# Kernel tuning notes

Measured on AMD Instinct MI355X. Metric: run time of the kernel, lower is better.

## Reference

```python
import jax, jax.numpy as jnp
import numpy as np

VOC = 32000
D = 512          # embedding_dim == hidden_dim
POS = 1024       # position_embeddings_count


def _layernorm(x, gamma, beta, eps=1e-5):
    mu = jnp.mean(x, axis=-1, keepdims=True)
    var = jnp.var(x, axis=-1, keepdims=True)
    return (x - mu) * jax.lax.rsqrt(var + eps) * gamma + beta


def setup_inputs() -> dict:
    key = jax.random.key(0)
    ks = jax.random.split(key, 7)
    inp = jax.random.randint(ks[0], (32, 1024), 0, VOC)
    word_emb = jax.random.normal(ks[1], (VOC, D), dtype=jnp.float32) * 0.02
    pos_emb = jax.random.normal(ks[2], (POS, D), dtype=jnp.float32) * 0.02
    gamma = jnp.ones((D,), dtype=jnp.float32)
    beta = jnp.zeros((D,), dtype=jnp.float32)
    # torch.rand -> uniform [0,1) init in the original Attention module
    Wk = jax.random.uniform(ks[3], (D, D), dtype=jnp.float32)
    Wq = jax.random.uniform(ks[4], (D, D), dtype=jnp.float32)
    Wv = jax.random.uniform(ks[5], (D, D), dtype=jnp.float32)
    return {"input": inp, "word_emb": word_emb, "pos_emb": pos_emb,
            "gamma": gamma, "beta": beta, "Wk": Wk, "Wq": Wq, "Wv": Wv}


def reference(input, word_emb, pos_emb, gamma, beta, Wk, Wq, Wv):
    S = input.shape[-1]
    # MiniBertEmbedding: word + positional, then LayerNorm
    emb = word_emb[input] + pos_emb[:S][None, :, :]   # [B,S,D]
    x = _layernorm(emb, gamma, beta)
    # Attention: single-head QK^T softmax V with param matrices
    k = jnp.einsum('bsd,dh->bsh', x, Wk)
    q = jnp.einsum('bsd,dh->bsh', x, Wq)
    v = jnp.einsum('bsd,do->bso', x, Wv)
    qk = jnp.einsum('bqh,bkh->bqk', q, k) / jnp.sqrt(jnp.float32(D))
    attn = jax.nn.softmax(qk, axis=-1)
    return jnp.einsum('bqk,bko->bqo', attn, v)
```

## Files before the change

### kernel.cpp

```cpp
#include <hip/hip_runtime.h>
#include <math.h>

typedef _Float16 f16;
typedef _Float16 half8 __attribute__((ext_vector_type(8)));
typedef _Float16 hv2 __attribute__((ext_vector_type(2)));
typedef _Float16 hv4 __attribute__((ext_vector_type(4)));
typedef float f32x4 __attribute__((ext_vector_type(4)));
typedef __attribute__((address_space(1))) const unsigned int gu32;
typedef __attribute__((address_space(3))) unsigned int lu32;

#define BB 32
#define SS 1024
#define DD 512
#define NR (BB*SS)
#define CH 16

__device__ __forceinline__ void stage128(const char* g, int ldb, char* lds,
                                         int wv, int ln) {
  #pragma unroll
  for (int r = 0; r < 4; r++) {
    int slot = r * 256 + wv * 64 + ln;
    int row = slot >> 3, cp = slot & 7;
    int c = cp ^ (row & 7);
    const char* gp = g + (size_t)row * ldb + (c << 4);
    char* lp = lds + ((slot - ln) << 4);
    __builtin_amdgcn_global_load_lds((gu32*)gp, (lu32*)lp, 16, 0, 0);
  }
}

__device__ __forceinline__ void stage8k_512(const char* g, int ldb, char* lds) {
  int tid = threadIdx.x;
  int slot = tid;
  int row = slot >> 3, cp = slot & 7;
  int c = cp ^ (row & 7);
  const char* gp = g + (size_t)row * ldb + (c << 4);
  char* lp = lds + ((slot - (tid & 63)) << 4);
  __builtin_amdgcn_global_load_lds((gu32*)gp, (lu32*)lp, 16, 0, 0);
}

__device__ __forceinline__ half8 frag_ld(const char* lds, int row, int kc) {
  return *(const half8*)(lds + row * 128 + ((kc ^ (row & 7)) << 4));
}

__device__ __forceinline__ f32x4 MF(half8 a, half8 b, f32x4 c) {
  return __builtin_amdgcn_mfma_f32_16x16x32_f16(a, b, c, 0, 0, 0);
}

__global__ __launch_bounds__(256) void k_prep(
    const int* __restrict__ inp, const float* __restrict__ wemb,
    const float* __restrict__ pemb, const float* __restrict__ gamma,
    const float* __restrict__ beta, f16* __restrict__ Xhi, f16* __restrict__ Xlo,
    const float* __restrict__ Wq, const float* __restrict__ Wk,
    const float* __restrict__ Wv, f16* __restrict__ Wqh, f16* __restrict__ Wql,
    f16* __restrict__ Wkh, f16* __restrict__ Wkl, f16* __restrict__ Wvt)
{
  int bid = blockIdx.x;
  int tid = threadIdx.x;
  __shared__ float red[10];
  __shared__ float Lt[64][65];
  if (bid >= NR) {
    int t  = bid - NR;
    int mz = t >> 6;
    int tt = t & 63;
    if (mz < 2) {
      const float* W = mz ? Wk : Wq;
      f16* Oh = mz ? Wkh : Wqh;
      f16* Ol = mz ? Wkl : Wql;
      #pragma unroll
      for (int p = 0; p < 4; p++) {
        size_t base = (size_t)tt * 4096 + p * 1024 + tid * 4;
        float4 v = *(const float4*)&W[base];
        f16 h0 = (f16)v.x, h1 = (f16)v.y, h2 = (f16)v.z, h3 = (f16)v.w;
        hv4 hi = {h0, h1, h2, h3};
        hv4 lo = {(f16)(v.x - (float)h0), (f16)(v.y - (float)h1),
                  (f16)(v.z - (float)h2), (f16)(v.w - (float)h3)};
        *(hv4*)&Oh[base] = hi;
        *(hv4*)&Ol[base] = lo;
      }
      return;
    }
    int tr = tt >> 3, tc = tt & 7;
    int rr = tid >> 4;
    int c4 = (tid & 15) * 4;
    #pragma unroll
    for (int p = 0; p < 4; p++) {
      float4 v = *(const float4*)&Wv[(size_t)(tr * 64 + p * 16 + rr) * DD + tc * 64 + c4];
      Lt[p * 16 + rr][c4 + 0] = v.x; Lt[p * 16 + rr][c4 + 1] = v.y;
      Lt[p * 16 + rr][c4 + 2] = v.z; Lt[p * 16 + rr][c4 + 3] = v.w;
    }
    __syncthreads();
    #pragma unroll
    for (int p = 0; p < 4; p++) {
      int dl = p * 16 + rr;
      float v0 = Lt[c4 + 0][dl], v1 = Lt[c4 + 1][dl];
      float v2 = Lt[c4 + 2][dl], v3 = Lt[c4 + 3][dl];
      size_t o = (size_t)(tc * 64 + dl) * DD + tr * 64 + c4;
      *(hv4*)&Wvt[o] = (hv4){(f16)v0, (f16)v1, (f16)v2, (f16)v3};
    }
    return;
  }
  int row = bid;
  int s   = row & (SS - 1);
  int tok = inp[row];
  float2 w = ((const float2*)(wemb + (size_t)tok * DD))[tid];
  float2 p = ((const float2*)(pemb + (size_t)s   * DD))[tid];
  float ex = w.x + p.x, ey = w.y + p.y;
  float sum = ex + ey, ssq = ex*ex + ey*ey;
  #pragma unroll
  for (int off = 32; off > 0; off >>= 1) {
    sum += __shfl_down(sum, off, 64);
    ssq += __shfl_down(ssq, off, 64);
  }
  int wv = tid >> 6, ln = tid & 63;
  if (ln == 0) { red[wv] = sum; red[4 + wv] = ssq; }
  __syncthreads();
  if (tid == 0) {
    float s4 = red[0] + red[1] + red[2] + red[3];
    float q4 = red[4] + red[5] + red[6] + red[7];
    float mean = s4 * (1.0f / DD);
    float var  = q4 * (1.0f / DD) - mean * mean;
    red[8] = mean; red[9] = rsqrtf(var + 1e-5f);
  }
  __syncthreads();
  float mean = red[8], rstd = red[9];
  float2 g  = ((const float2*)gamma)[tid];
  float2 bt = ((const float2*)beta)[tid];
  float ox = (ex - mean) * rstd * g.x + bt.x;
  float oy = (ey - mean) * rstd * g.y + bt.y;
  f16 hx = (f16)ox, hy = (f16)oy;
  f16 lx = (f16)(ox - (float)hx), ly = (f16)(oy - (float)hy);
  ((hv2*)(Xhi + (size_t)row * DD))[tid] = (hv2){hx, hy};
  ((hv2*)(Xlo + (size_t)row * DD))[tid] = (hv2){lx, ly};
}

__global__ __launch_bounds__(256, 2) void k_mt(
    const f16* __restrict__ Wkh, const f16* __restrict__ Wkl,
    const f16* __restrict__ Wqh, const f16* __restrict__ Wql,
    f16* __restrict__ Mthi, f16* __restrict__ Mtlo)
{
  __shared__ __align__(16) char Ah[16384], Al[16384], Bh[16384], Bl[16384];
  int tid = threadIdx.x, wv = tid >> 6, ln = tid & 63;
  int mw = wv & 1, nw = wv >> 1;
  int n0 = blockIdx.x * 128;
  int m0 = blockIdx.y * 128;
  f32x4 acc[4][4];
  #pragma unroll
  for (int i = 0; i < 4; i++)
    #pragma unroll
    for (int j = 0; j < 4; j++) acc[i][j] = (f32x4)(0.0f);
  int quad = ln >> 4, l15 = ln & 15;
  for (int k0 = 0; k0 < DD; k0 += 64) {
    __syncthreads();
    stage128((const char*)(Wkh + (size_t)m0 * DD + k0), 1024, Ah, wv, ln);
    stage128((const char*)(Wkl + (size_t)m0 * DD + k0), 1024, Al, wv, ln);
    stage128((const char*)(Wqh + (size_t)n0 * DD + k0), 1024, Bh, wv, ln);
    stage128((const char*)(Wql + (size_t)n0 * DD + k0), 1024, Bl, wv, ln);
    __syncthreads();
    #pragma unroll
    for (int ks = 0; ks < 2; ks++) {
      int kc = ks * 4 + quad;
      half8 ah[4], al[4], bh[4], bl[4];
      #pragma unroll
      for (int t = 0; t < 4; t++) {
        ah[t] = frag_ld(Ah, mw * 64 + t * 16 + l15, kc);
        al[t] = frag_ld(Al, mw * 64 + t * 16 + l15, kc);
        bh[t] = frag_ld(Bh, nw * 64 + t * 16 + l15, kc);
        bl[t] = frag_ld(Bl, nw * 64 + t * 16 + l15, kc);
      }
      #pragma unroll
      for (int i = 0; i < 4; i++)
        #pragma unroll
        for (int j = 0; j < 4; j++) {
          acc[i][j] = MF(ah[i], bh[j], acc[i][j]);
          acc[i][j] = MF(ah[i], bl[j], acc[i][j]);
          acc[i][j] = MF(al[i], bh[j], acc[i][j]);
        }
    }
  }
  #pragma unroll
  for (int i = 0; i < 4; i++)
    #pragma unroll
    for (int j = 0; j < 4; j++)
      #pragma unroll
      for (int rg = 0; rg < 4; rg++) {
        int gm = m0 + mw * 64 + i * 16 + quad * 4 + rg;
        int gn = n0 + nw * 64 + j * 16 + l15;
        size_t o = (size_t)gm * DD + gn;
        float v = acc[i][j][rg];
        f16 h = (f16)v;
        Mthi[o] = h; Mtlo[o] = (f16)(v - (float)h);
      }
}

__global__ __launch_bounds__(256, 2) void k_projm(
    const f16* __restrict__ Xhi, const f16* __restrict__ Xlo,
    const f16* __restrict__ Mthi, const f16* __restrict__ Mtlo,
    f16* __restrict__ Sqhi, f16* __restrict__ Sqlo)
{
  __shared__ __align__(16) char Ah[16384], Al[16384], Bh[16384], Bl[16384];
  int tid = threadIdx.x, wv = tid >> 6, ln = tid & 63;
  int mw = wv & 1, nw = wv >> 1;
  int L = blockIdx.x;
  int xb = (L >> 3) & 3;
  int y  = ((L >> 5) << 3) + (L & 7);
  int n0 = xb * 128;
  int m0 = y * 128;
  f32x4 acc[4][4];
  #pragma unroll
  for (int i = 0; i < 4; i++)
    #pragma unroll
    for (int j = 0; j < 4; j++) acc[i][j] = (f32x4)(0.0f);
  int quad = ln >> 4, l15 = ln & 15;
  for (int k0 = 0; k0 < DD; k0 += 64) {
    __syncthreads();
    stage128((const char*)(Xhi  + (size_t)m0 * DD + k0), 1024, Ah, wv, ln);
    stage128((const char*)(Xlo  + (size_t)m0 * DD + k0), 1024, Al, wv, ln);
    stage128((const char*)(Mthi + (size_t)n0 * DD + k0), 1024, Bh, wv, ln);
    stage128((const char*)(Mtlo + (size_t)n0 * DD + k0), 1024, Bl, wv, ln);
    __syncthreads();
    #pragma unroll
    for (int ks = 0; ks < 2; ks++) {
      int kc = ks * 4 + quad;
      half8 ah[4], al[4], bh[4], bl[4];
      #pragma unroll
      for (int t = 0; t < 4; t++) {
        ah[t] = frag_ld(Ah, mw * 64 + t * 16 + l15, kc);
        al[t] = frag_ld(Al, mw * 64 + t * 16 + l15, kc);
        bh[t] = frag_ld(Bh, nw * 64 + t * 16 + l15, kc);
        bl[t] = frag_ld(Bl, nw * 64 + t * 16 + l15, kc);
      }
      #pragma unroll
      for (int i = 0; i < 4; i++)
        #pragma unroll
        for (int j = 0; j < 4; j++) {
          acc[i][j] = MF(ah[i], bh[j], acc[i][j]);
          acc[i][j] = MF(ah[i], bl[j], acc[i][j]);
          acc[i][j] = MF(al[i], bh[j], acc[i][j]);
        }
    }
  }
  #pragma unroll
  for (int i = 0; i < 4; i++)
    #pragma unroll
    for (int j = 0; j < 4; j++)
      #pragma unroll
      for (int rg = 0; rg < 4; rg++) {
        int gm = m0 + mw * 64 + i * 16 + quad * 4 + rg;
        int gn = n0 + nw * 64 + j * 16 + l15;
        size_t o = (size_t)gm * DD + gn;
        float v = acc[i][j][rg];
        f16 h = (f16)v;
        Sqhi[o] = h; Sqlo[o] = (f16)(v - (float)h);
      }
}

__global__ __launch_bounds__(256, 2) void k_vt(
    const f16* __restrict__ Wvt, const f16* __restrict__ Xhi, f16* __restrict__ Vt)
{
  __shared__ __align__(16) char Ah[16384], Bh[16384];
  int tid = threadIdx.x, wv = tid >> 6, ln = tid & 63;
  int mw = wv & 1, nw = wv >> 1;
  int n0 = blockIdx.x * 128;
  int m0 = blockIdx.y * 128;
  f32x4 acc[4][4];
  #pragma unroll
  for (int i = 0; i < 4; i++)
    #pragma unroll
    for (int j = 0; j < 4; j++) acc[i][j] = (f32x4)(0.0f);
  for (int k0 = 0; k0 < DD; k0 += 64) {
    __syncthreads();
    stage128((const char*)(Wvt + (size_t)m0 * DD + k0), 1024, Ah, wv, ln);
    stage128((const char*)(Xhi + (size_t)n0 * DD + k0), 1024, Bh, wv, ln);
    __syncthreads();
    int quad = ln >> 4, l15 = ln & 15;
    #pragma unroll
    for (int ks = 0; ks < 2; ks++) {
      int kc = ks * 4 + quad;
      half8 a[4], b[4];
      #pragma unroll
      for (int t = 0; t < 4; t++) {
        a[t] = frag_ld(Ah, mw * 64 + t * 16 + l15, kc);
        b[t] = frag_ld(Bh, nw * 64 + t * 16 + l15, kc);
      }
      #pragma unroll
      for (int i = 0; i < 4; i++)
        #pragma unroll
        for (int j = 0; j < 4; j++) acc[i][j] = MF(a[i], b[j], acc[i][j]);
    }
  }
  int quad = ln >> 4, l15 = ln & 15;
  #pragma unroll
  for (int i = 0; i < 4; i++)
    #pragma unroll
    for (int j = 0; j < 4; j++)
      #pragma unroll
      for (int rg = 0; rg < 4; rg++) {
        int gm = m0 + mw * 64 + i * 16 + quad * 4 + rg;
        int gn = n0 + nw * 64 + j * 16 + l15;
        Vt[(size_t)gm * NR + gn] = (f16)acc[i][j][rg];
      }
}

__global__ __launch_bounds__(512, 2) void k_qk(
    const f16* __restrict__ Sqhi, const f16* __restrict__ Sqlo,
    const f16* __restrict__ Xhi, const f16* __restrict__ Xlo,
    f16* __restrict__ Pws, f16* __restrict__ Pd)
{
  __shared__ __align__(16) char Ah[8192], Al[8192];
  __shared__ __align__(16) char Bh[2][4][8192], Bl[2][4][8192];
  __shared__ float redm[4][64], reds[4][64];
  int tid = threadIdx.x, wv = tid >> 6, ln = tid & 63;
  int rowg = wv & 1, qd = wv >> 1;
  int L = blockIdx.x;
  int g  = L >> 7;
  int rr = L & 127;
  int z  = g * 8 + (rr & 7);
  int m0 = (rr >> 3) * 64;
  size_t zr = (size_t)z * SS;
  f32x4 acc[2][16];
  #pragma unroll
  for (int i = 0; i < 2; i++)
    #pragma unroll
    for (int j = 0; j < 16; j++) acc[i][j] = (f32x4)(0.0f);
  int quad = ln >> 4, l15 = ln & 15;

  #pragma unroll
  for (int q4 = 0; q4 < 4; q4++) {
    stage8k_512((const char*)(Xhi + (zr + q4 * 256) * DD), 1024, Bh[0][q4]);
    stage8k_512((const char*)(Xlo + (zr + q4 * 256) * DD), 1024, Bl[0][q4]);
  }

  for (int k0 = 0; k0 < DD; k0 += 64) {
    #pragma unroll
    for (int r = 0; r < 4; r++) {
      __builtin_amdgcn_s_barrier();
      __builtin_amdgcn_sched_barrier(0);
      if (r == 0) {
        stage8k_512((const char*)(Sqhi + (zr + m0) * DD + k0), 1024, Ah);
        stage8k_512((const char*)(Sqlo + (zr + m0) * DD + k0), 1024, Al);
      }
      bool haveNext = !(k0 == DD - 64 && r == 3);
      if (haveNext) {
        int nk0 = (r == 3) ? k0 + 64 : k0;
        int nr  = (r + 1) & 3;
        #pragma unroll
        for (int q4 = 0; q4 < 4; q4++) {
          int n0 = q4 * 256 + nr * 64;
          stage8k_512((const char*)(Xhi + (zr + n0) * DD + nk0), 1024, Bh[(r + 1) & 1][q4]);
          stage8k_512((const char*)(Xlo + (zr + n0) * DD + nk0), 1024, Bl[(r + 1) & 1][q4]);
        }
        asm volatile("s_waitcnt vmcnt(8)" ::: "memory");
      } else {
        asm volatile("s_waitcnt vmcnt(0)" ::: "memory");
      }
      __builtin_amdgcn_s_barrier();
      __builtin_amdgcn_sched_barrier(0);
      #pragma unroll
      for (int ks = 0; ks < 2; ks++) {
        int kc = ks * 4 + quad;
        half8 ah[2], al[2];
        #pragma unroll
        for (int i = 0; i < 2; i++) {
          ah[i] = frag_ld(Ah, rowg * 32 + i * 16 + l15, kc);
          al[i] = frag_ld(Al, rowg * 32 + i * 16 + l15, kc);
        }
        #pragma unroll
        for (int jj = 0; jj < 4; jj++) {
          half8 bh = frag_ld(Bh[r & 1][qd], jj * 16 + l15, kc);
          half8 bl = frag_ld(Bl[r & 1][qd], jj * 16 + l15, kc);
          #pragma unroll
          for (int i = 0; i < 2; i++) {
            acc[i][r * 4 + jj] = MF(ah[i], bh, acc[i][r * 4 + jj]);
            acc[i][r * 4 + jj] = MF(ah[i], bl, acc[i][r * 4 + jj]);
            acc[i][r * 4 + jj] = MF(al[i], bh, acc[i][r * 4 + jj]);
          }
        }
      }
    }
  }

  const float scale = 0.044194173824159216f;
  float mx[2][4];
  #pragma unroll
  for (int i = 0; i < 2; i++)
    #pragma unroll
    for (int rg = 0; rg < 4; rg++) mx[i][rg] = -3.0e38f;
  #pragma unroll
  for (int i = 0; i < 2; i++)
    #pragma unroll
    for (int j = 0; j < 16; j++)
      #pragma unroll
      for (int rg = 0; rg < 4; rg++) {
        acc[i][j][rg] *= scale;
        mx[i][rg] = fmaxf(mx[i][rg], acc[i][j][rg]);
      }
  #pragma unroll
  for (int off = 1; off < 16; off <<= 1)
    #pragma unroll
    for (int i = 0; i < 2; i++)
      #pragma unroll
      for (int rg = 0; rg < 4; rg++)
        mx[i][rg] = fmaxf(mx[i][rg], __shfl_xor(mx[i][rg], off, 64));
  if (l15 == 0) {
    #pragma unroll
    for (int i = 0; i < 2; i++)
      #pragma unroll
      for (int rg = 0; rg < 4; rg++)
        redm[qd][rowg * 32 + i * 16 + quad * 4 + rg] = mx[i][rg];
  }
  __syncthreads();
  float fm[2][4], sum[2][4];
  #pragma unroll
  for (int i = 0; i < 2; i++)
    #pragma unroll
    for (int rg = 0; rg < 4; rg++) {
      int row = rowg * 32 + i * 16 + quad * 4 + rg;
      fm[i][rg] = fmaxf(fmaxf(redm[0][row], redm[1][row]),
                        fmaxf(redm[2][row], redm[3][row]));
      sum[i][rg] = 0.0f;
    }
  #pragma unroll
  for (int i = 0; i < 2; i++)
    #pragma unroll
    for (int j = 0; j < 16; j++)
      #pragma unroll
      for (int rg = 0; rg < 4; rg++) {
        float e = __expf(acc[i][j][rg] - fm[i][rg]);
        acc[i][j][rg] = e;
        sum[i][rg] += e;
      }
  #pragma unroll
  for (int off = 1; off < 16; off <<= 1)
    #pragma unroll
    for (int i = 0; i < 2; i++)
      #pragma unroll
      for (int rg = 0; rg < 4; rg++)
        sum[i][rg] += __shfl_xor(sum[i][rg], off, 64);
  if (l15 == 0) {
    #pragma unroll
    for (int i = 0; i < 2; i++)
      #pragma unroll
      for (int rg = 0; rg < 4; rg++)
        reds[qd][rowg * 32 + i * 16 + quad * 4 + rg] = sum[i][rg];
  }
  __syncthreads();
  float inv[2][4];
  #pragma unroll
  for (int i = 0; i < 2; i++)
    #pragma unroll
    for (int rg = 0; rg < 4; rg++) {
      int row = rowg * 32 + i * 16 + quad * 4 + rg;
      inv[i][rg] = 1.0f / (reds[0][row] + reds[1][row] + reds[2][row] + reds[3][row]);
    }
  f16* Pb = (z < CH) ? Pws : Pd;
  size_t zo = (size_t)((z < CH) ? z : z - CH);
  #pragma unroll
  for (int i = 0; i < 2; i++)
    #pragma unroll
    for (int j = 0; j < 16; j++)
      #pragma unroll
      for (int rg = 0; rg < 4; rg++) {
        int row = rowg * 32 + i * 16 + quad * 4 + rg;
        int col = qd * 256 + j * 16 + l15;
        Pb[(zo * SS + m0 + row) * SS + col] = (f16)(acc[i][j][rg] * inv[i][rg]);
      }
}

__global__ __launch_bounds__(256, 2) void k_pv(
    const f16* __restrict__ P, const f16* __restrict__ Vt, float* __restrict__ O,
    int zoff)
{
  __shared__ __align__(16) char Ah[16384], Bh[16384];
  int tid = threadIdx.x, wv = tid >> 6, ln = tid & 63;
  int mw = wv & 1, nw = wv >> 1;
  int n0 = blockIdx.x * 128;
  int m0 = blockIdx.y * 128;
  int zl = blockIdx.z;
  int b  = zoff + zl;
  const char* Pt = (const char*)(P + ((size_t)zl * SS + m0) * SS);
  f32x4 acc[4][4];
  #pragma unroll
  for (int i = 0; i < 4; i++)
    #pragma unroll
    for (int j = 0; j < 4; j++) acc[i][j] = (f32x4)(0.0f);
  for (int k0 = 0; k0 < SS; k0 += 64) {
    __syncthreads();
    stage128(Pt + k0 * 2, 2048, Ah, wv, ln);
    stage128((const char*)(Vt + (size_t)n0 * NR + (size_t)b * SS + k0), NR * 2, Bh, wv, ln);
    __syncthreads();
    int quad = ln >> 4, l15 = ln & 15;
    #pragma unroll
    for (int ks = 0; ks < 2; ks++) {
      int kc = ks * 4 + quad;
      half8 a[4], bf[4];
      #pragma unroll
      for (int t = 0; t < 4; t++) {
        a[t]  = frag_ld(Ah, mw * 64 + t * 16 + l15, kc);
        bf[t] = frag_ld(Bh, nw * 64 + t * 16 + l15, kc);
      }
      #pragma unroll
      for (int i = 0; i < 4; i++)
        #pragma unroll
        for (int j = 0; j < 4; j++) acc[i][j] = MF(a[i], bf[j], acc[i][j]);
    }
  }
  int quad = ln >> 4, l15 = ln & 15;
  #pragma unroll
  for (int i = 0; i < 4; i++)
    #pragma unroll
    for (int j = 0; j < 4; j++)
      #pragma unroll
      for (int rg = 0; rg < 4; rg++) {
        int gm = m0 + mw * 64 + i * 16 + quad * 4 + rg;
        int gn = n0 + nw * 64 + j * 16 + l15;
        O[((size_t)b * SS + gm) * DD + gn] = acc[i][j][rg];
      }
}

extern "C" void kernel_launch(void* const* d_in, const int* in_sizes, int n_in,
                              void* d_out, int out_size, void* d_ws, size_t ws_size,
                              hipStream_t stream) {
  const int*   inp   = (const int*)d_in[0];
  const float* wemb  = (const float*)d_in[1];
  const float* pemb  = (const float*)d_in[2];
  const float* gamma = (const float*)d_in[3];
  const float* beta  = (const float*)d_in[4];
  const float* Wk    = (const float*)d_in[5];
  const float* Wq    = (const float*)d_in[6];
  const float* Wv    = (const float*)d_in[7];

  char* ws = (char*)d_ws;
  f16* Xhi  = (f16*)ws;
  f16* Xlo  = (f16*)(ws + ((size_t)32 << 20));
  f16* Sqhi = (f16*)(ws + ((size_t)64 << 20));
  f16* Sqlo = (f16*)(ws + ((size_t)96 << 20));
  f16* Vt   = (f16*)(ws + ((size_t)128 << 20));
  f16* Pws  = (f16*)(ws + ((size_t)160 << 20));
  f16* Pd   = (f16*)d_out;

  f16* Wqh  = (f16*)d_out;
  f16* Wql  = Wqh + (size_t)DD * DD;
  f16* Wkh  = Wql + (size_t)DD * DD;
  f16* Wkl  = Wkh + (size_t)DD * DD;
  f16* Wvt  = Wkl + (size_t)DD * DD;
  f16* Mthi = Wvt + (size_t)DD * DD;
  f16* Mtlo = Mthi + (size_t)DD * DD;

  k_prep<<<NR + 192, 256, 0, stream>>>(inp, wemb, pemb, gamma, beta, Xhi, Xlo,
                                       Wq, Wk, Wv, Wqh, Wql, Wkh, Wkl, Wvt);
  k_mt<<<dim3(DD / 128, DD / 128), 256, 0, stream>>>(Wkh, Wkl, Wqh, Wql, Mthi, Mtlo);
  k_projm<<<1024, 256, 0, stream>>>(Xhi, Xlo, Mthi, Mtlo, Sqhi, Sqlo);
  k_vt<<<dim3(NR / 128, DD / 128), 256, 0, stream>>>(Wvt, Xhi, Vt);
  k_qk<<<512, 512, 0, stream>>>(Sqhi, Sqlo, Xhi, Xlo, Pws, Pd);
  k_pv<<<dim3(DD / 128, SS / 128, CH), 256, 0, stream>>>(Pd,  Vt, (float*)d_out, CH);
  k_pv<<<dim3(DD / 128, SS / 128, CH), 256, 0, stream>>>(Pws, Vt, (float*)d_out, 0);
}
```

Measured before the change: 424.4 us.

## Double-buffer LDS in k_vt/k_pv, remap blocks per XCD, hoist A fragments in k_qk

```diff
diff --git a/kernel.cpp b/kernel.cpp
--- a/kernel.cpp
+++ b/kernel.cpp
@@ -257,30 +257,43 @@
 __global__ __launch_bounds__(256, 2) void k_vt(
     const f16* __restrict__ Wvt, const f16* __restrict__ Xhi, f16* __restrict__ Vt)
 {
-  __shared__ __align__(16) char Ah[16384], Bh[16384];
+  __shared__ __align__(16) char Ah[2][16384], Bh[2][16384];
   int tid = threadIdx.x, wv = tid >> 6, ln = tid & 63;
   int mw = wv & 1, nw = wv >> 1;
-  int n0 = blockIdx.x * 128;
-  int m0 = blockIdx.y * 128;
+  int orig = blockIdx.x;
+  int L = (orig & 7) * 128 + (orig >> 3);
+  int c = L >> 7, t = L & 127;
+  int m0 = (t & 3) * 128;
+  int n0 = (c * 32 + (t >> 2)) * 128;
   f32x4 acc[4][4];
   #pragma unroll
   for (int i = 0; i < 4; i++)
     #pragma unroll
     for (int j = 0; j < 4; j++) acc[i][j] = (f32x4)(0.0f);
+  int quad = ln >> 4, l15 = ln & 15;
+  stage128((const char*)(Wvt + (size_t)m0 * DD), 1024, Ah[0], wv, ln);
+  stage128((const char*)(Xhi + (size_t)n0 * DD), 1024, Bh[0], wv, ln);
   for (int k0 = 0; k0 < DD; k0 += 64) {
-    __syncthreads();
-    stage128((const char*)(Wvt + (size_t)m0 * DD + k0), 1024, Ah, wv, ln);
-    stage128((const char*)(Xhi + (size_t)n0 * DD + k0), 1024, Bh, wv, ln);
-    __syncthreads();
-    int quad = ln >> 4, l15 = ln & 15;
+    int cur = (k0 >> 6) & 1;
+    __builtin_amdgcn_s_barrier();
+    __builtin_amdgcn_sched_barrier(0);
+    if (k0 + 64 < DD) {
+      stage128((const char*)(Wvt + (size_t)m0 * DD + k0 + 64), 1024, Ah[cur ^ 1], wv, ln);
+      stage128((const char*)(Xhi + (size_t)n0 * DD + k0 + 64), 1024, Bh[cur ^ 1], wv, ln);
+      asm volatile("s_waitcnt vmcnt(8)" ::: "memory");
+    } else {
+      asm volatile("s_waitcnt vmcnt(0)" ::: "memory");
+    }
+    __builtin_amdgcn_s_barrier();
+    __builtin_amdgcn_sched_barrier(0);
     #pragma unroll
     for (int ks = 0; ks < 2; ks++) {
       int kc = ks * 4 + quad;
       half8 a[4], b[4];
       #pragma unroll
-      for (int t = 0; t < 4; t++) {
-        a[t] = frag_ld(Ah, mw * 64 + t * 16 + l15, kc);
-        b[t] = frag_ld(Bh, nw * 64 + t * 16 + l15, kc);
+      for (int tt = 0; tt < 4; tt++) {
+        a[tt] = frag_ld(Ah[cur], mw * 64 + tt * 16 + l15, kc);
+        b[tt] = frag_ld(Bh[cur], nw * 64 + tt * 16 + l15, kc);
       }
       #pragma unroll
       for (int i = 0; i < 4; i++)
@@ -288,7 +301,6 @@
         for (int j = 0; j < 4; j++) acc[i][j] = MF(a[i], b[j], acc[i][j]);
     }
   }
-  int quad = ln >> 4, l15 = ln & 15;
   #pragma unroll
   for (int i = 0; i < 4; i++)
     #pragma unroll
@@ -330,6 +342,7 @@
     stage8k_512((const char*)(Xlo + (zr + q4 * 256) * DD), 1024, Bl[0][q4]);
   }
 
+  half8 afh[2][2], afl[2][2];
   for (int k0 = 0; k0 < DD; k0 += 64) {
     #pragma unroll
     for (int r = 0; r < 4; r++) {
@@ -355,24 +368,27 @@
       }
       __builtin_amdgcn_s_barrier();
       __builtin_amdgcn_sched_barrier(0);
+      if (r == 0) {
+        #pragma unroll
+        for (int ks = 0; ks < 2; ks++)
+          #pragma unroll
+          for (int i = 0; i < 2; i++) {
+            afh[ks][i] = frag_ld(Ah, rowg * 32 + i * 16 + l15, ks * 4 + quad);
+            afl[ks][i] = frag_ld(Al, rowg * 32 + i * 16 + l15, ks * 4 + quad);
+          }
+      }
       #pragma unroll
       for (int ks = 0; ks < 2; ks++) {
         int kc = ks * 4 + quad;
-        half8 ah[2], al[2];
-        #pragma unroll
-        for (int i = 0; i < 2; i++) {
-          ah[i] = frag_ld(Ah, rowg * 32 + i * 16 + l15, kc);
-          al[i] = frag_ld(Al, rowg * 32 + i * 16 + l15, kc);
-        }
         #pragma unroll
         for (int jj = 0; jj < 4; jj++) {
           half8 bh = frag_ld(Bh[r & 1][qd], jj * 16 + l15, kc);
           half8 bl = frag_ld(Bl[r & 1][qd], jj * 16 + l15, kc);
           #pragma unroll
           for (int i = 0; i < 2; i++) {
-            acc[i][r * 4 + jj] = MF(ah[i], bh, acc[i][r * 4 + jj]);
-            acc[i][r * 4 + jj] = MF(ah[i], bl, acc[i][r * 4 + jj]);
-            acc[i][r * 4 + jj] = MF(al[i], bh, acc[i][r * 4 + jj]);
+            acc[i][r * 4 + jj] = MF(afh[ks][i], bh, acc[i][r * 4 + jj]);
+            acc[i][r * 4 + jj] = MF(afh[ks][i], bl, acc[i][r * 4 + jj]);
+            acc[i][r * 4 + jj] = MF(afl[ks][i], bh, acc[i][r * 4 + jj]);
           }
         }
       }
@@ -470,33 +486,47 @@
     const f16* __restrict__ P, const f16* __restrict__ Vt, float* __restrict__ O,
     int zoff)
 {
-  __shared__ __align__(16) char Ah[16384], Bh[16384];
+  __shared__ __align__(16) char Ah[2][16384], Bh[2][16384];
   int tid = threadIdx.x, wv = tid >> 6, ln = tid & 63;
   int mw = wv & 1, nw = wv >> 1;
-  int n0 = blockIdx.x * 128;
-  int m0 = blockIdx.y * 128;
-  int zl = blockIdx.z;
+  int orig = blockIdx.x;
+  int L = (orig & 7) * 64 + (orig >> 3);
+  int c = L >> 6, t = L & 63;
+  int zl = 2 * c + (t >> 5);
+  int m0 = ((t >> 2) & 7) * 128;
+  int n0 = (t & 3) * 128;
   int b  = zoff + zl;
   const char* Pt = (const char*)(P + ((size_t)zl * SS + m0) * SS);
+  const char* Vb = (const char*)(Vt + (size_t)n0 * NR + (size_t)b * SS);
   f32x4 acc[4][4];
   #pragma unroll
   for (int i = 0; i < 4; i++)
     #pragma unroll
     for (int j = 0; j < 4; j++) acc[i][j] = (f32x4)(0.0f);
+  int quad = ln >> 4, l15 = ln & 15;
+  stage128(Pt, 2048, Ah[0], wv, ln);
+  stage128(Vb, NR * 2, Bh[0], wv, ln);
   for (int k0 = 0; k0 < SS; k0 += 64) {
-    __syncthreads();
-    stage128(Pt + k0 * 2, 2048, Ah, wv, ln);
-    stage128((const char*)(Vt + (size_t)n0 * NR + (size_t)b * SS + k0), NR * 2, Bh, wv, ln);
-    __syncthreads();
-    int quad = ln >> 4, l15 = ln & 15;
+    int cur = (k0 >> 6) & 1;
+    __builtin_amdgcn_s_barrier();
+    __builtin_amdgcn_sched_barrier(0);
+    if (k0 + 64 < SS) {
+      stage128(Pt + (k0 + 64) * 2, 2048, Ah[cur ^ 1], wv, ln);
+      stage128(Vb + (k0 + 64) * 2, NR * 2, Bh[cur ^ 1], wv, ln);
+      asm volatile("s_waitcnt vmcnt(8)" ::: "memory");
+    } else {
+      asm volatile("s_waitcnt vmcnt(0)" ::: "memory");
+    }
+    __builtin_amdgcn_s_barrier();
+    __builtin_amdgcn_sched_barrier(0);
     #pragma unroll
     for (int ks = 0; ks < 2; ks++) {
       int kc = ks * 4 + quad;
       half8 a[4], bf[4];
       #pragma unroll
-      for (int t = 0; t < 4; t++) {
-        a[t]  = frag_ld(Ah, mw * 64 + t * 16 + l15, kc);
-        bf[t] = frag_ld(Bh, nw * 64 + t * 16 + l15, kc);
+      for (int tt = 0; tt < 4; tt++) {
+        a[tt]  = frag_ld(Ah[cur], mw * 64 + tt * 16 + l15, kc);
+        bf[tt] = frag_ld(Bh[cur], nw * 64 + tt * 16 + l15, kc);
       }
       #pragma unroll
       for (int i = 0; i < 4; i++)
@@ -504,7 +534,6 @@
         for (int j = 0; j < 4; j++) acc[i][j] = MF(a[i], bf[j], acc[i][j]);
     }
   }
-  int quad = ln >> 4, l15 = ln & 15;
   #pragma unroll
   for (int i = 0; i < 4; i++)
     #pragma unroll
@@ -550,8 +579,8 @@
                                        Wq, Wk, Wv, Wqh, Wql, Wkh, Wkl, Wvt);
   k_mt<<<dim3(DD / 128, DD / 128), 256, 0, stream>>>(Wkh, Wkl, Wqh, Wql, Mthi, Mtlo);
   k_projm<<<1024, 256, 0, stream>>>(Xhi, Xlo, Mthi, Mtlo, Sqhi, Sqlo);
-  k_vt<<<dim3(NR / 128, DD / 128), 256, 0, stream>>>(Wvt, Xhi, Vt);
+  k_vt<<<1024, 256, 0, stream>>>(Wvt, Xhi, Vt);
   k_qk<<<512, 512, 0, stream>>>(Sqhi, Sqlo, Xhi, Xlo, Pws, Pd);
-  k_pv<<<dim3(DD / 128, SS / 128, CH), 256, 0, stream>>>(Pd,  Vt, (float*)d_out, CH);
-  k_pv<<<dim3(DD / 128, SS / 128, CH), 256, 0, stream>>>(Pws, Vt, (float*)d_out, 0);
-}
+  k_pv<<<512, 256, 0, stream>>>(Pd,  Vt, (float*)d_out, CH);
+  k_pv<<<512, 256, 0, stream>>>(Pws, Vt, (float*)d_out, 0);
+}
```

Result: no change. 425.1 us (+0.2%).
